# Performance work log

Measured on AMD Instinct MI355X. Metric: run time of the kernel, lower is better.

Reference implementation:

```python
import jax, jax.numpy as jnp
import numpy as np

# --- static architecture constants (from tokenizer / module defaults) ---
SIZES = np.array([5, 15, 5] + [34] * 16)
STOPS = np.cumsum(SIZES)                    # seq_stop_position
N_ALLELE = 16
SEG_LEN = 5 + 15 + 5 + 34                   # 59: nflank+peptide+cflank+one mhc
D_MODEL = 256                               # node_feat_size
K_CAND = 8                                  # binding-core candidates per (allele,sample) graph
VOCAB = 30
NEG_FILL = -1000.0


def sinusoidal_pe(length, dim):
    pos = jnp.arange(length, dtype=jnp.float32)[:, None]
    div = jnp.exp(jnp.arange(0, dim, 2, dtype=jnp.float32) * (-jnp.log(10000.0) / dim))
    pe = jnp.zeros((length, dim), dtype=jnp.float32)
    pe = pe.at[:, 0::2].set(jnp.sin(pos * div))
    pe = pe.at[:, 1::2].set(jnp.cos(pos * div))
    return pe


def setup_inputs() -> dict:
    key = jax.random.key(0)
    k1, k2, k3, k4, k5 = jax.random.split(key, 5)
    B = 512
    L = int(STOPS[-1])  # 569
    x_data = jax.random.randint(k1, (B, L), 0, VOCAB, dtype=jnp.int64)
    emb = jax.random.normal(k2, (VOCAB, D_MODEL), dtype=jnp.float32) * 0.02
    emb = emb.at[0].set(0.0)  # padding_idx=0
    # surrogate graph-scorer params (stand-in for DGL AttentiveFP GNN+readout+predict)
    W_pool = jax.random.normal(k3, (K_CAND, SEG_LEN), dtype=jnp.float32) * 0.1
    W_pred = jax.random.normal(k4, (D_MODEL,), dtype=jnp.float32) * 0.05
    b_pred = jax.random.normal(k5, (), dtype=jnp.float32) * 0.01
    return {"x_data": x_data, "emb": emb, "W_pool": W_pool, "W_pred": W_pred, "b_pred": b_pred}


def reference(x_data, emb, W_pool, W_pred, b_pred):
    B = x_data.shape[0]
    G = N_ALLELE * B
    # --- slice into segments (static stop positions) ---
    common = x_data[:, :STOPS[2]]                                     # [B, 25]
    mhc = [x_data[:, STOPS[i + 2]:STOPS[i + 3]] for i in range(N_ALLELE)]
    # feat_full_token: cat over alleles of (common, mhc_i) -> [16B, 59]
    feat_tok = jnp.concatenate(
        [jnp.concatenate([common, m], axis=1) for m in mhc], axis=0)
    mask_full = (feat_tok != 0)                                       # valid positions
    # --- embedding + positional encoding + mask ---
    feat = emb[feat_tok]                                              # [16B, 59, D]
    feat = feat + sinusoidal_pe(SEG_LEN, D_MODEL)[None]               # posenc (eval: no dropout)
    feat = feat * mask_full[..., None].astype(feat.dtype)
    # --- allele presence (first token of each mhc block nonzero) ---
    presence = jnp.concatenate([m[:, 0] != 0 for m in mhc], axis=0)   # [16B]
    # --- surrogate per-candidate graph scores (K candidates per entry) ---
    cand = jnp.einsum('nld,kl->nkd', feat, W_pool)                    # [16B, K, D]
    preds = jnp.einsum('nkd,d->nk', cand, W_pred) + b_pred            # [16B, K]
    # --- segment max / argmax over candidate groups (the torch.unique loop) ---
    # segments are contiguous groups of K; index = repeat(arange(16B), K)
    seg_max = jnp.max(preds, axis=1)                                  # [16B]
    seg_arg = jnp.argmax(preds, axis=1)                               # [16B]
    # --- scatter back into full (allele, sample) grid with fill values ---
    preds_full = jnp.where(presence, seg_max, NEG_FILL).reshape(N_ALLELE, B)
    gidx_full = jnp.where(presence, seg_arg, -1).reshape(N_ALLELE, B)
    # eval-mode output: cat along allele dim then transpose -> [B, 32]
    out = jnp.concatenate([preds_full, gidx_full.astype(preds_full.dtype)], axis=0)
    return jnp.transpose(out, (1, 0))
```

## Files before the change

kernel.cpp:

```cpp
#include <hip/hip_runtime.h>

#define BATCH    512
#define L_TOT    569
#define NALLELE  16
#define SEG_LEN  59
#define D_MODEL  256
#define K_CAND   8
#define VOCAB    30
#define COMMON   25
#define NEG_FILL -1000.0f

__global__ __launch_bounds__(256) void mhc_pool_kernel(
    const int*   __restrict__ x,
    const float* __restrict__ emb,
    const float* __restrict__ wpool,
    const float* __restrict__ wpred,
    const float* __restrict__ bpred,
    float*       __restrict__ out)
{
    __shared__ float s_edot[VOCAB];
    __shared__ float s_pedot[60];
    __shared__ float s_wpT[60][8];

    const int t = threadIdx.x;
    const int h = t & 3;
    const int g = blockIdx.x * 64 + (t >> 2);
    const int i = g & (NALLELE - 1);
    const int b = g >> 4;
    const int rowbase = b * L_TOT;

    int toks[15];
    #pragma unroll
    for (int q = 0; q < 15; ++q) {
        const int l = 15 * h + q;
        const int addr = (l < COMMON) ? (rowbase + l)
                       : (l < SEG_LEN) ? (rowbase + 34 * i + l)
                                       : rowbase;
        toks[q] = x[addr];
    }
    const int tok0 = (h == 0) ? x[rowbase + COMMON + 34 * i] : 0;

    const float c0 = -0.035977892f;
    if (t < 120) {
        const int j = t >> 2, q = t & 3;
        const float4* e = reinterpret_cast<const float4*>(emb + j * D_MODEL + q * 64);
        const float4* w = reinterpret_cast<const float4*>(wpred + q * 64);
        float a0 = 0, a1 = 0, a2 = 0, a3 = 0;
        #pragma unroll
        for (int p = 0; p < 16; ++p) {
            const float4 ev = e[p], wv = w[p];
            a0 = fmaf(ev.x, wv.x, a0);
            a1 = fmaf(ev.y, wv.y, a1);
            a2 = fmaf(ev.z, wv.z, a2);
            a3 = fmaf(ev.w, wv.w, a3);
        }
        float part = (a0 + a1) + (a2 + a3);
        part += __shfl_xor(part, 1);
        part += __shfl_xor(part, 2);
        if (q == 0) s_edot[j] = part;
    } else if (t < 238) {
        const int tt = t - 120;
        const int j = tt >> 1, q = tt & 1;
        const float pos = (float)j;
        float       dv  = q ? __expf(c0 * 64.0f) : 1.0f;
        const float r   = __expf(c0 * 2.0f);
        float a0 = 0.0f, a1 = 0.0f;
        #pragma unroll
        for (int p = 0; p < 32; ++p) {
            const float2 wv  = reinterpret_cast<const float2*>(wpred)[32 * q + p];
            const float  ang = pos * dv;
            a0 = fmaf(__sinf(ang), wv.x, a0);
            a1 = fmaf(__cosf(ang), wv.y, a1);
            dv *= r;
        }
        float part = a0 + a1;
        part += __shfl_xor(part, 1);
        if (q == 0) s_pedot[j] = part;
        if (tt == 116) s_pedot[59] = 0.0f;
    }
    for (int idx = t; idx < 480; idx += 256) {
        const int l = idx >> 3, k = idx & 7;
        s_wpT[l][k] = (l < SEG_LEN) ? wpool[k * SEG_LEN + l] : 0.0f;
    }
    __syncthreads();

    float acc[K_CAND] = {0, 0, 0, 0, 0, 0, 0, 0};
    #pragma unroll
    for (int q = 0; q < 15; ++q) {
        const int   l   = 15 * h + q;
        const int   tok = toks[q];
        const float s   = (tok != 0) ? (s_edot[tok] + s_pedot[l]) : 0.0f;
        const float4 wlo = *reinterpret_cast<const float4*>(&s_wpT[l][0]);
        const float4 whi = *reinterpret_cast<const float4*>(&s_wpT[l][4]);
        acc[0] = fmaf(wlo.x, s, acc[0]);
        acc[1] = fmaf(wlo.y, s, acc[1]);
        acc[2] = fmaf(wlo.z, s, acc[2]);
        acc[3] = fmaf(wlo.w, s, acc[3]);
        acc[4] = fmaf(whi.x, s, acc[4]);
        acc[5] = fmaf(whi.y, s, acc[5]);
        acc[6] = fmaf(whi.z, s, acc[6]);
        acc[7] = fmaf(whi.w, s, acc[7]);
    }

    #pragma unroll
    for (int k = 0; k < K_CAND; ++k) {
        acc[k] += __shfl_xor(acc[k], 1);
        acc[k] += __shfl_xor(acc[k], 2);
    }

    if (h == 0) {
        float bv = acc[0]; int bk = 0;
        #pragma unroll
        for (int k = 1; k < K_CAND; ++k)
            if (acc[k] > bv) { bv = acc[k]; bk = k; }
        const bool pres = (tok0 != 0);
        out[b * 32 + i]           = pres ? (bv + bpred[0]) : NEG_FILL;
        out[b * 32 + NALLELE + i] = pres ? (float)bk       : -1.0f;
    }
}

extern "C" void kernel_launch(void* const* d_in, const int* in_sizes, int n_in,
                              void* d_out, int out_size, void* d_ws, size_t ws_size,
                              hipStream_t stream) {
    const int*   x     = (const int*)  d_in[0];
    const float* emb   = (const float*)d_in[1];
    const float* wpool = (const float*)d_in[2];
    const float* wpred = (const float*)d_in[3];
    const float* bpred = (const float*)d_in[4];
    float*       out   = (float*)d_out;

    mhc_pool_kernel<<<128, 256, 0, stream>>>(x, emb, wpool, wpred, bpred, out);
}
```

Before: 10.90 us.

## Stage token rows in shared memory and split work across more blocks

Each block now cooperatively loads two full token rows into shared memory with coalesced reads, replacing the scattered per-thread gathers from global memory. Eight threads now share each (allele, sample) pair instead of four, so each block covers 32 pairs and the grid doubles to 256 blocks, giving more parallelism across CUs. The cost is that every block recomputes the embedding and positional dot tables, twice as many blocks in total, plus an extra shuffle stage in the reduction.

Result: slower. 11.36 us (+4.2%).

```diff
diff --git a/kernel.cpp b/kernel.cpp
--- a/kernel.cpp
+++ b/kernel.cpp
@@ -18,27 +18,18 @@
     const float* __restrict__ bpred,
     float*       __restrict__ out)
 {
+    __shared__ int   s_x[2 * L_TOT];
     __shared__ float s_edot[VOCAB];
-    __shared__ float s_pedot[60];
-    __shared__ float s_wpT[60][8];
+    __shared__ float s_pedot[64];
+    __shared__ float s_wpT[64][8];
 
     const int t = threadIdx.x;
-    const int h = t & 3;
-    const int g = blockIdx.x * 64 + (t >> 2);
-    const int i = g & (NALLELE - 1);
-    const int b = g >> 4;
-    const int rowbase = b * L_TOT;
 
-    int toks[15];
-    #pragma unroll
-    for (int q = 0; q < 15; ++q) {
-        const int l = 15 * h + q;
-        const int addr = (l < COMMON) ? (rowbase + l)
-                       : (l < SEG_LEN) ? (rowbase + 34 * i + l)
-                                       : rowbase;
-        toks[q] = x[addr];
+    {
+        const int base = blockIdx.x * (2 * L_TOT);
+        for (int idx = t; idx < 2 * L_TOT; idx += 256)
+            s_x[idx] = x[base + idx];
     }
-    const int tok0 = (h == 0) ? x[rowbase + COMMON + 34 * i] : 0;
 
     const float c0 = -0.035977892f;
     if (t < 120) {
@@ -76,20 +67,31 @@
         float part = a0 + a1;
         part += __shfl_xor(part, 1);
         if (q == 0) s_pedot[j] = part;
-        if (tt == 116) s_pedot[59] = 0.0f;
+    } else if (t < 243) {
+        s_pedot[59 + (t - 238)] = 0.0f;
     }
-    for (int idx = t; idx < 480; idx += 256) {
+    for (int idx = t; idx < 512; idx += 256) {
         const int l = idx >> 3, k = idx & 7;
         s_wpT[l][k] = (l < SEG_LEN) ? wpool[k * SEG_LEN + l] : 0.0f;
     }
     __syncthreads();
 
+    const int  pr = t >> 3;
+    const int  h  = t & 7;
+    const int  g  = blockIdx.x * 32 + pr;
+    const int  i  = g & (NALLELE - 1);
+    const int  b  = g >> 4;
+    const int* srow = s_x + (pr >> 4) * L_TOT;
+
     float acc[K_CAND] = {0, 0, 0, 0, 0, 0, 0, 0};
     #pragma unroll
-    for (int q = 0; q < 15; ++q) {
-        const int   l   = 15 * h + q;
-        const int   tok = toks[q];
-        const float s   = (tok != 0) ? (s_edot[tok] + s_pedot[l]) : 0.0f;
+    for (int q = 0; q < 8; ++q) {
+        const int l   = 8 * h + q;
+        const int off = (l < COMMON) ? l
+                      : (l < SEG_LEN) ? (34 * i + l)
+                                      : 0;
+        const int tok = srow[off];
+        const float s = (tok != 0) ? (s_edot[tok] + s_pedot[l]) : 0.0f;
         const float4 wlo = *reinterpret_cast<const float4*>(&s_wpT[l][0]);
         const float4 whi = *reinterpret_cast<const float4*>(&s_wpT[l][4]);
         acc[0] = fmaf(wlo.x, s, acc[0]);
@@ -106,6 +108,7 @@
     for (int k = 0; k < K_CAND; ++k) {
         acc[k] += __shfl_xor(acc[k], 1);
         acc[k] += __shfl_xor(acc[k], 2);
+        acc[k] += __shfl_xor(acc[k], 4);
     }
 
     if (h == 0) {
@@ -113,7 +116,7 @@
         #pragma unroll
         for (int k = 1; k < K_CAND; ++k)
             if (acc[k] > bv) { bv = acc[k]; bk = k; }
-        const bool pres = (tok0 != 0);
+        const bool pres = (srow[COMMON + 34 * i] != 0);
         out[b * 32 + i]           = pres ? (bv + bpred[0]) : NEG_FILL;
         out[b * 32 + NALLELE + i] = pres ? (float)bk       : -1.0f;
     }
@@ -129,5 +132,5 @@
     const float* bpred = (const float*)d_in[4];
     float*       out   = (float*)d_out;
 
-    mhc_pool_kernel<<<128, 256, 0, stream>>>(x, emb, wpool, wpred, bpred, out);
+    mhc_pool_kernel<<<256, 256, 0, stream>>>(x, emb, wpool, wpred, bpred, out);
 }
```
